# Performance work log

Hardware: AMD Instinct MI355X
Metric: run time of the kernel (lower is better)

Reference implementation:

```python
import jax, jax.numpy as jnp
import numpy as np

N_EMBD = 1024
N_HEAD = 16
B, T = 1, 4096
EPS = 1e-5


def layer_norm(x, w):
    mu = jnp.mean(x, axis=-1, keepdims=True)
    var = jnp.var(x, axis=-1, keepdims=True)
    return (x - mu) / jnp.sqrt(var + EPS) * w


def setup_inputs() -> dict:
    key = jax.random.key(0)
    ks = jax.random.split(key, 6)
    s = 0.02
    return {
        "x": jax.random.normal(ks[0], (B, T, N_EMBD), dtype=jnp.float32),
        "w_qkv": jax.random.normal(ks[1], (N_EMBD, 3 * N_EMBD), dtype=jnp.float32) * s,
        "w_attn_proj": jax.random.normal(ks[2], (N_EMBD, N_EMBD), dtype=jnp.float32) * s,
        "w_fc": jax.random.normal(ks[3], (N_EMBD, 4 * N_EMBD), dtype=jnp.float32) * s,
        "w_mlp_proj": jax.random.normal(ks[4], (4 * N_EMBD, N_EMBD), dtype=jnp.float32) * s,
        "ln1_w": jnp.ones((N_EMBD,), dtype=jnp.float32),
        "ln2_w": jnp.ones((N_EMBD,), dtype=jnp.float32),
    }


def reference(x, w_qkv, w_attn_proj, w_fc, w_mlp_proj, ln1_w, ln2_w):
    Bq, Tq, C = x.shape
    hs = C // N_HEAD

    # --- attention branch (pre-norm) ---
    h = layer_norm(x, ln1_w)
    qkv = h @ w_qkv  # [B,T,3C]
    q, k, v = jnp.split(qkv, 3, axis=-1)
    q = q.reshape(Bq, Tq, N_HEAD, hs).transpose(0, 2, 1, 3)  # [B,H,T,hs]
    k = k.reshape(Bq, Tq, N_HEAD, hs).transpose(0, 2, 1, 3)
    v = v.reshape(Bq, Tq, N_HEAD, hs).transpose(0, 2, 1, 3)

    scores = jnp.einsum("bhqd,bhkd->bhqk", q, k) * (1.0 / jnp.sqrt(jnp.float32(hs)))
    causal = jnp.tril(jnp.ones((Tq, Tq), dtype=bool))
    scores = jnp.where(causal, scores, -jnp.inf)
    weights = jax.nn.softmax(scores, axis=-1)  # dropout=0 -> identity
    out = jnp.einsum("bhqk,bhkd->bhqd", weights, v)
    out = out.transpose(0, 2, 1, 3).reshape(Bq, Tq, C)
    x = x + out @ w_attn_proj

    # --- MLP branch (pre-norm) ---
    h = layer_norm(x, ln2_w)
    h = jax.nn.gelu(h @ w_fc, approximate=False)  # nn.GELU default is exact
    x = x + h @ w_mlp_proj
    return x
```

## Files before the change

### kernel.cpp

```cpp
#include <hip/hip_runtime.h>
#include <cstdint>

typedef __attribute__((ext_vector_type(8))) short short8;
typedef __attribute__((ext_vector_type(4))) float f32x4;

__device__ __forceinline__ float b2f(unsigned short u) {
    return __uint_as_float(((unsigned int)u) << 16);
}
__device__ __forceinline__ unsigned short f2b(float f) {
    unsigned int u = __float_as_uint(f);
    u += 0x7FFFu + ((u >> 16) & 1u);
    return (unsigned short)(u >> 16);
}
__device__ __forceinline__ void gload16(const unsigned short* g, unsigned short* l) {
    __builtin_amdgcn_global_load_lds(
        (const __attribute__((address_space(1))) void*)g,
        (__attribute__((address_space(3))) void*)l, 16, 0, 0);
}

__global__ __launch_bounds__(256) void k_transpose_all(
        const float* __restrict__ w0, const float* __restrict__ w1,
        const float* __restrict__ w2, const float* __restrict__ w3,
        unsigned short* __restrict__ o0, unsigned short* __restrict__ o1,
        unsigned short* __restrict__ o2, unsigned short* __restrict__ o3) {
    __shared__ float tile[32][33];
    int b = blockIdx.x;
    const float* w; unsigned short* o; int K, N, nx, tb;
    if (b < 3072)      { w = w0; o = o0; K = 1024; N = 3072; nx = 96;  tb = b; }
    else if (b < 4096) { w = w1; o = o1; K = 1024; N = 1024; nx = 32;  tb = b - 3072; }
    else if (b < 8192) { w = w2; o = o2; K = 1024; N = 4096; nx = 128; tb = b - 4096; }
    else               { w = w3; o = o3; K = 4096; N = 1024; nx = 32;  tb = b - 8192; }
    int n0 = (tb % nx) * 32, k0 = (tb / nx) * 32;
    int tx = threadIdx.x, ty = threadIdx.y;
#pragma unroll
    for (int i = 0; i < 4; i++)
        tile[ty + 8 * i][tx] = w[(size_t)(k0 + ty + 8 * i) * N + n0 + tx];
    __syncthreads();
#pragma unroll
    for (int i = 0; i < 4; i++)
        o[(size_t)(n0 + ty + 8 * i) * K + k0 + tx] = f2b(tile[tx][ty + 8 * i]);
}

__global__ __launch_bounds__(256) void k_layernorm(
        const float* __restrict__ x, const float* __restrict__ w,
        unsigned short* __restrict__ out) {
    int row = blockIdx.x, tid = threadIdx.x;
    const float4* xr = (const float4*)(x + (size_t)row * 1024);
    float4 v = xr[tid];
    float s  = v.x + v.y + v.z + v.w;
    float ss = v.x * v.x + v.y * v.y + v.z * v.z + v.w * v.w;
#pragma unroll
    for (int off = 32; off >= 1; off >>= 1) {
        s  += __shfl_down(s, off);
        ss += __shfl_down(ss, off);
    }
    __shared__ float red[10];
    if ((tid & 63) == 0) { red[tid >> 6] = s; red[4 + (tid >> 6)] = ss; }
    __syncthreads();
    if (tid == 0) {
        float S  = red[0] + red[1] + red[2] + red[3];
        float SS = red[4] + red[5] + red[6] + red[7];
        float mu  = S * (1.0f / 1024.0f);
        float var = SS * (1.0f / 1024.0f) - mu * mu;
        red[8] = mu; red[9] = rsqrtf(var + 1e-5f);
    }
    __syncthreads();
    float mu = red[8], rs = red[9];
    float4 wv = ((const float4*)w)[tid];
    ushort4 pk;
    pk.x = f2b((v.x - mu) * rs * wv.x);
    pk.y = f2b((v.y - mu) * rs * wv.y);
    pk.z = f2b((v.z - mu) * rs * wv.z);
    pk.w = f2b((v.w - mu) * rs * wv.w);
    *(ushort4*)(out + (size_t)row * 1024 + tid * 4) = pk;
}

__global__ __launch_bounds__(256) void k_reduce_ln(
        const float* __restrict__ res, const float* __restrict__ p0,
        const float* __restrict__ p1, const float* __restrict__ w,
        float* __restrict__ xout, unsigned short* __restrict__ hout) {
    int row = blockIdx.x, tid = threadIdx.x;
    size_t i = (size_t)row * 256 + tid;
    float4 a = ((const float4*)res)[i];
    float4 b = ((const float4*)p0)[i];
    float4 c = ((const float4*)p1)[i];
    float4 v;
    v.x = a.x + b.x + c.x; v.y = a.y + b.y + c.y;
    v.z = a.z + b.z + c.z; v.w = a.w + b.w + c.w;
    ((float4*)xout)[i] = v;
    float s  = v.x + v.y + v.z + v.w;
    float ss = v.x * v.x + v.y * v.y + v.z * v.z + v.w * v.w;
#pragma unroll
    for (int off = 32; off >= 1; off >>= 1) {
        s  += __shfl_down(s, off);
        ss += __shfl_down(ss, off);
    }
    __shared__ float red[10];
    if ((tid & 63) == 0) { red[tid >> 6] = s; red[4 + (tid >> 6)] = ss; }
    __syncthreads();
    if (tid == 0) {
        float S  = red[0] + red[1] + red[2] + red[3];
        float SS = red[4] + red[5] + red[6] + red[7];
        float mu  = S * (1.0f / 1024.0f);
        float var = SS * (1.0f / 1024.0f) - mu * mu;
        red[8] = mu; red[9] = rsqrtf(var + 1e-5f);
    }
    __syncthreads();
    float mu = red[8], rs = red[9];
    float4 wv = ((const float4*)w)[tid];
    ushort4 pk;
    pk.x = f2b((v.x - mu) * rs * wv.x);
    pk.y = f2b((v.y - mu) * rs * wv.y);
    pk.z = f2b((v.z - mu) * rs * wv.z);
    pk.w = f2b((v.w - mu) * rs * wv.w);
    *(ushort4*)(hout + (size_t)row * 1024 + tid * 4) = pk;
}

__global__ __launch_bounds__(256) void k_reduce(
        const float* __restrict__ res, const float* __restrict__ p0,
        const float* __restrict__ p1, float* __restrict__ out, int n4) {
    int i = blockIdx.x * 256 + threadIdx.x;
    if (i < n4) {
        float4 a = ((const float4*)res)[i];
        float4 b = ((const float4*)p0)[i];
        float4 c = ((const float4*)p1)[i];
        a.x += b.x + c.x; a.y += b.y + c.y; a.z += b.z + c.z; a.w += b.w + c.w;
        ((float4*)out)[i] = a;
    }
}

template <int EPI, int TM, int TN, int MINW>
__global__ __launch_bounds__(256, MINW) void k_gemm_bt(
        const unsigned short* __restrict__ A, const unsigned short* __restrict__ BT,
        const float* __restrict__ RES, void* __restrict__ OUT,
        int M, int N, int K) {
    constexpr int WT = (TM == 128) ? 64 : 32;
    constexpr int MI = WT / 16;
    constexpr int NA = TM / 32, NB = TN / 32;
    __shared__ __align__(16) unsigned short As[TM * 64];
    __shared__ __align__(16) unsigned short Bs[TN * 64];
    int tid  = threadIdx.x;
    int lane = tid & 63, wave = tid >> 6;
    int quad = lane >> 4, qr = lane & 15;
    int wm_off = (wave >> 1) * WT;
    int wn_off = (wave & 1) * WT;
    int m0 = blockIdx.y * TM, n0 = blockIdx.x * TN;
    int ks = K / gridDim.z;
    int kbeg = blockIdx.z * ks;
    int r0 = tid >> 3;
    int c0 = (tid & 7) * 8;
    int cs = 8 * (((tid & 7) + (r0 & 7)) & 7);
    int cswz[2];
#pragma unroll
    for (int kk = 0; kk < 2; kk++) cswz[kk] = 8 * (((kk * 4) + quad + (qr & 7)) & 7);

    const unsigned short* Ap = A  + (size_t)(m0 + r0) * K + kbeg + c0;
    const unsigned short* Bp = BT + (size_t)(n0 + r0) * K + kbeg + c0;
    const size_t sA = (size_t)32 * K;

    uint4 pa0, pa1, pa2, pa3, pb0, pb1, pb2, pb3;
    pa0 = *(const uint4*)(Ap);
    pa1 = *(const uint4*)(Ap + sA);
    if constexpr (NA == 4) {
        pa2 = *(const uint4*)(Ap + 2 * sA);
        pa3 = *(const uint4*)(Ap + 3 * sA);
    }
    pb0 = *(const uint4*)(Bp);
    pb1 = *(const uint4*)(Bp + sA);
    if constexpr (NB == 4) {
        pb2 = *(const uint4*)(Bp + 2 * sA);
        pb3 = *(const uint4*)(Bp + 3 * sA);
    }

    f32x4 acc[MI][MI] = {};
    for (int k0 = 0; k0 < ks; k0 += 64) {
        __syncthreads();
        *(uint4*)&As[(r0)      * 64 + cs] = pa0;
        *(uint4*)&As[(32 + r0) * 64 + cs] = pa1;
        if constexpr (NA == 4) {
            *(uint4*)&As[(64 + r0) * 64 + cs] = pa2;
            *(uint4*)&As[(96 + r0) * 64 + cs] = pa3;
        }
        *(uint4*)&Bs[(r0)      * 64 + cs] = pb0;
        *(uint4*)&Bs[(32 + r0) * 64 + cs] = pb1;
        if constexpr (NB == 4) {
            *(uint4*)&Bs[(64 + r0) * 64 + cs] = pb2;
            *(uint4*)&Bs[(96 + r0) * 64 + cs] = pb3;
        }
        __syncthreads();
        if (k0 + 64 < ks) {
            int k = k0 + 64;
            pa0 = *(const uint4*)(Ap + k);
            pa1 = *(const uint4*)(Ap + sA + k);
            if constexpr (NA == 4) {
                pa2 = *(const uint4*)(Ap + 2 * sA + k);
                pa3 = *(const uint4*)(Ap + 3 * sA + k);
            }
            pb0 = *(const uint4*)(Bp + k);
            pb1 = *(const uint4*)(Bp + sA + k);
            if constexpr (NB == 4) {
                pb2 = *(const uint4*)(Bp + 2 * sA + k);
                pb3 = *(const uint4*)(Bp + 3 * sA + k);
            }
        }
#pragma unroll
        for (int kk = 0; kk < 2; kk++) {
            short8 af[MI], bfr[MI];
#pragma unroll
            for (int i = 0; i < MI; i++) af[i]  = *(const short8*)&As[(wm_off + i * 16 + qr) * 64 + cswz[kk]];
#pragma unroll
            for (int j = 0; j < MI; j++) bfr[j] = *(const short8*)&Bs[(wn_off + j * 16 + qr) * 64 + cswz[kk]];
#pragma unroll
            for (int i = 0; i < MI; i++)
#pragma unroll
                for (int j = 0; j < MI; j++)
                    acc[i][j] = __builtin_amdgcn_mfma_f32_16x16x32_bf16(af[i], bfr[j], acc[i][j], 0, 0, 0);
        }
    }
    float* outz = (EPI == 0) ? ((float*)OUT + (size_t)blockIdx.z * M * N) : (float*)OUT;
#pragma unroll
    for (int i = 0; i < MI; i++) {
#pragma unroll
        for (int j = 0; j < MI; j++) {
#pragma unroll
            for (int r = 0; r < 4; r++) {
                int row = m0 + wm_off + i * 16 + quad * 4 + r;
                int col = n0 + wn_off + j * 16 + qr;
                size_t idx = (size_t)row * N + col;
                float v = acc[i][j][r];
                if (EPI == 0)      outz[idx] = v;
                else if (EPI == 1) ((unsigned short*)OUT)[idx] = f2b(v);
                else if (EPI == 2) ((float*)OUT)[idx] = RES[idx] + v;
                else {
                    float u = v * fmaf(v * v, 0.035677408f, 0.79788456f);
                    float e = fminf(u * 2.885390082f, 80.0f);
                    float t = exp2f(e);
                    float g = v * t / (t + 1.0f);
                    ((unsigned short*)OUT)[idx] = f2b(g);
                }
            }
        }
    }
}

template <int EPI>
__global__ __launch_bounds__(512, 2) void k_gemm_8p(
        const unsigned short* __restrict__ A, const unsigned short* __restrict__ BT,
        void* __restrict__ OUT, int M, int N, int K) {
    __shared__ __align__(16) unsigned short As[2][256 * 64];
    __shared__ __align__(16) unsigned short Bs[2][256 * 64];
    int tid = threadIdx.x;
    int lane = tid & 63, wave = tid >> 6;
    int quad = lane >> 4, qr = lane & 15;
    int wr = wave >> 2, wc = wave & 3;
    int m0 = blockIdx.y * 256, n0 = blockIdx.x * 256;
    int nk = K / 64;

    int srow = tid >> 3, sblk = tid & 7;
    int scol = 8 * ((sblk - (srow & 7)) & 7);
    const unsigned short* Ag = A  + (size_t)(m0 + srow) * K + scol;
    const unsigned short* Bg = BT + (size_t)(n0 + srow) * K + scol;
    const size_t rstep = (size_t)64 * K;

    int cswz[2];
#pragma unroll
    for (int kk = 0; kk < 2; kk++) cswz[kk] = 8 * (((kk * 4) + quad + (qr & 7)) & 7);

    auto stageA = [&](int buf, int half, int kt) {
        int k = (kt < nk ? kt : 0) * 64;
#pragma unroll
        for (int rr = 0; rr < 2; rr++) {
            int r4 = half * 2 + rr;
            gload16(Ag + (size_t)r4 * rstep + k, &As[buf][r4 * 4096 + wave * 512]);
        }
    };
    auto stageB = [&](int buf, int half, int kt) {
        int k = (kt < nk ? kt : 0) * 64;
#pragma unroll
        for (int rr = 0; rr < 2; rr++) {
            int r4 = half * 2 + rr;
            gload16(Bg + (size_t)r4 * rstep + k, &Bs[buf][r4 * 4096 + wave * 512]);
        }
    };

    f32x4 acc[8][4] = {};
    stageA(0, 0, 0); stageA(0, 1, 0); stageB(0, 0, 0); stageB(0, 1, 0);
    stageA(1, 0, 1); stageA(1, 1, 1); stageB(1, 0, 1); stageB(1, 1, 1);
    asm volatile("s_waitcnt vmcnt(8)" ::: "memory");
    __builtin_amdgcn_s_barrier();

    short8 bf[4][2];
    for (int t = 0; t < nk; t += 2) {
#pragma unroll
        for (int ph = 0; ph < 8; ph++) {
            const int B = ph >> 2;
            const int p = ph & 3;
            if (p == 0) {
#pragma unroll
                for (int j = 0; j < 4; j++)
#pragma unroll
                    for (int kk = 0; kk < 2; kk++)
                        bf[j][kk] = *(const short8*)&Bs[B][(wc * 64 + j * 16 + qr) * 64 + cswz[kk]];
            }
            short8 af[2][2];
#pragma unroll
            for (int i2 = 0; i2 < 2; i2++)
#pragma unroll
                for (int kk = 0; kk < 2; kk++)
                    af[i2][kk] = *(const short8*)&As[B][(wr * 128 + (p * 2 + i2) * 16 + qr) * 64 + cswz[kk]];
            if (ph == 0)      { if (t) stageA(1, 0, t + 1); }
            else if (ph == 1) { if (t) stageA(1, 1, t + 1); stageB(0, 0, t + 2); }
            else if (ph == 2) { stageB(0, 1, t + 2); }
            else if (ph == 4) { stageA(0, 0, t + 2); }
            else if (ph == 5) { stageA(0, 1, t + 2); stageB(1, 0, t + 3); }
            else if (ph == 6) { stageB(1, 1, t + 3); }
            __builtin_amdgcn_s_barrier();
            asm volatile("s_waitcnt lgkmcnt(0)" ::: "memory");
            __builtin_amdgcn_sched_barrier(0);
            __builtin_amdgcn_s_setprio(1);
#pragma unroll
            for (int i2 = 0; i2 < 2; i2++)
#pragma unroll
                for (int kk = 0; kk < 2; kk++)
#pragma unroll
                    for (int j = 0; j < 4; j++)
                        acc[p * 2 + i2][j] = __builtin_amdgcn_mfma_f32_16x16x32_bf16(
                            af[i2][kk], bf[j][kk], acc[p * 2 + i2][j], 0, 0, 0);
            __builtin_amdgcn_s_setprio(0);
            if (p == 3) asm volatile("s_waitcnt vmcnt(4)" ::: "memory");
            __builtin_amdgcn_s_barrier();
        }
    }
    asm volatile("s_waitcnt vmcnt(0)" ::: "memory");

#pragma unroll
    for (int i = 0; i < 8; i++) {
#pragma unroll
        for (int j = 0; j < 4; j++) {
#pragma unroll
            for (int r = 0; r < 4; r++) {
                int row = m0 + wr * 128 + i * 16 + quad * 4 + r;
                int col = n0 + wc * 64 + j * 16 + qr;
                size_t idx = (size_t)row * N + col;
                float v = acc[i][j][r];
                if (EPI == 1) ((unsigned short*)OUT)[idx] = f2b(v);
                else {
                    float u = v * fmaf(v * v, 0.035677408f, 0.79788456f);
                    float e = fminf(u * 2.885390082f, 80.0f);
                    float tt = exp2f(e);
                    float g = v * tt / (tt + 1.0f);
                    ((unsigned short*)OUT)[idx] = f2b(g);
                }
            }
        }
    }
}

__global__ __launch_bounds__(256) void k_attn(
        const unsigned short* __restrict__ qkv, unsigned short* __restrict__ out) {
    __shared__ unsigned short Ks[128][72];
    __shared__ unsigned short Vt[64][136];
    __shared__ unsigned short Ps[4][16][136];

    const float C1 = 0.18033688f;
    const float C2 = 5.77078016f;

    int l = blockIdx.x;
    int h = l & 15;
    int qb = 63 - (l >> 4);
    int q0 = qb * 64;

    int tid = threadIdx.x;
    int wave = tid >> 6, lane = tid & 63;
    int lane16 = lane & 15, quad = lane >> 4;

    {
        int srow = tid >> 2, sc0 = (tid & 3) * 16;
        size_t base = (size_t)(q0 + srow) * 3072 + h * 64 + sc0;
        *(uint4*)&Ks[srow][sc0]     = *(const uint4*)&qkv[base];
        *(uint4*)&Ks[srow][sc0 + 8] = *(const uint4*)&qkv[base + 8];
    }
    __syncthreads();
    short8 aq0 = *(const short8*)&Ks[wave * 16 + lane16][quad * 8];
    short8 aq1 = *(const short8*)&Ks[wave * 16 + lane16][32 + quad * 8];

    f32x4 Oacc[4] = {};
    float l_part[4] = {0.f, 0.f, 0.f, 0.f};

    int srow = tid >> 1, sc0 = (tid & 1) * 32;
    int vk = (lane & 31) * 2;
    int d0 = wave * 16 + (lane >> 5) * 8;

    uint4 pk0, pk1, pk2, pk3, pv0, pv1, pv2, pv3;
    {
        size_t base = (size_t)srow * 3072 + 1024 + h * 64 + sc0;
        pk0 = *(const uint4*)&qkv[base];
        pk1 = *(const uint4*)&qkv[base + 8];
        pk2 = *(const uint4*)&qkv[base + 16];
        pk3 = *(const uint4*)&qkv[base + 24];
        size_t vb0 = (size_t)vk * 3072 + 2048 + h * 64 + d0;
        pv0 = *(const uint4*)&qkv[vb0];
        pv1 = *(const uint4*)&qkv[vb0 + 3072];
        size_t vb1 = (size_t)(64 + vk) * 3072 + 2048 + h * 64 + d0;
        pv2 = *(const uint4*)&qkv[vb1];
        pv3 = *(const uint4*)&qkv[vb1 + 3072];
    }

    for (int kc = 0; kc <= qb; kc += 2) {
        __syncthreads();
        {
            *(uint4*)&Ks[srow][sc0]      = pk0;
            *(uint4*)&Ks[srow][sc0 + 8]  = pk1;
            *(uint4*)&Ks[srow][sc0 + 16] = pk2;
            *(uint4*)&Ks[srow][sc0 + 24] = pk3;
        }
        {
            const unsigned short* pe0 = (const unsigned short*)&pv0;
            const unsigned short* po0 = (const unsigned short*)&pv1;
            const unsigned short* pe1 = (const unsigned short*)&pv2;
            const unsigned short* po1 = (const unsigned short*)&pv3;
#pragma unroll
            for (int j = 0; j < 8; j++) {
                *(uint32_t*)&Vt[d0 + j][vk]      = (uint32_t)pe0[j] | ((uint32_t)po0[j] << 16);
                *(uint32_t*)&Vt[d0 + j][64 + vk] = (uint32_t)pe1[j] | ((uint32_t)po1[j] << 16);
            }
        }
        __syncthreads();

        if (kc + 2 <= qb) {
            size_t base = (size_t)((kc + 2) * 64 + srow) * 3072 + 1024 + h * 64 + sc0;
            pk0 = *(const uint4*)&qkv[base];
            pk1 = *(const uint4*)&qkv[base + 8];
            pk2 = *(const uint4*)&qkv[base + 16];
            pk3 = *(const uint4*)&qkv[base + 24];
            size_t vb0 = (size_t)((kc + 2) * 64 + vk) * 3072 + 2048 + h * 64 + d0;
            pv0 = *(const uint4*)&qkv[vb0];
            pv1 = *(const uint4*)&qkv[vb0 + 3072];
            size_t vb1 = (size_t)((kc + 3) * 64 + vk) * 3072 + 2048 + h * 64 + d0;
            pv2 = *(const uint4*)&qkv[vb1];
            pv3 = *(const uint4*)&qkv[vb1 + 3072];
        }

        f32x4 sacc[8] = {};
#pragma unroll
        for (int kt = 0; kt < 8; kt++) {
            short8 bk0 = *(const short8*)&Ks[kt * 16 + lane16][quad * 8];
            short8 bk1 = *(const short8*)&Ks[kt * 16 + lane16][32 + quad * 8];
            sacc[kt] = __builtin_amdgcn_mfma_f32_16x16x32_bf16(aq0, bk0, sacc[kt], 0, 0, 0);
            sacc[kt] = __builtin_amdgcn_mfma_f32_16x16x32_bf16(aq1, bk1, sacc[kt], 0, 0, 0);
        }

        bool domask = (kc + 2 > qb);
#pragma unroll
        for (int r = 0; r < 4; r++) {
            int qrow = q0 + wave * 16 + quad * 4 + r;
#pragma unroll
            for (int kt = 0; kt < 8; kt++) {
                float s = sacc[kt][r];
                if (domask) {
                    int key = kc * 64 + kt * 16 + lane16;
                    s = (key <= qrow) ? s : -__builtin_inff();
                }
                float p = exp2f(fmaf(s, C1, -C2));
                l_part[r] += p;
                Ps[wave][quad * 4 + r][kt * 16 + lane16] =
                    (unsigned short)(__float_as_uint(p) >> 16);
            }
        }

#pragma unroll
        for (int s = 0; s < 4; s++) {
            short8 ap = *(const short8*)&Ps[wave][lane16][s * 32 + quad * 8];
#pragma unroll
            for (int dt = 0; dt < 4; dt++) {
                short8 bv = *(const short8*)&Vt[dt * 16 + lane16][s * 32 + quad * 8];
                Oacc[dt] = __builtin_amdgcn_mfma_f32_16x16x32_bf16(ap, bv, Oacc[dt], 0, 0, 0);
            }
        }
    }

    float invl[4];
#pragma unroll
    for (int r = 0; r < 4; r++) {
        float lf = l_part[r];
        lf += __shfl_xor(lf, 1);
        lf += __shfl_xor(lf, 2);
        lf += __shfl_xor(lf, 4);
        lf += __shfl_xor(lf, 8);
        invl[r] = 1.0f / lf;
    }
#pragma unroll
    for (int dt = 0; dt < 4; dt++) {
#pragma unroll
        for (int r = 0; r < 4; r++) {
            int qrow = q0 + wave * 16 + quad * 4 + r;
            out[(size_t)qrow * 1024 + h * 64 + dt * 16 + lane16] = f2b(Oacc[dt][r] * invl[r]);
        }
    }
}

extern "C" void kernel_launch(void* const* d_in, const int* in_sizes, int n_in,
                              void* d_out, int out_size, void* d_ws, size_t ws_size,
                              hipStream_t stream) {
    const float* x      = (const float*)d_in[0];
    const float* w_qkv  = (const float*)d_in[1];
    const float* w_attn = (const float*)d_in[2];
    const float* w_fc   = (const float*)d_in[3];
    const float* w_mlp  = (const float*)d_in[4];
    const float* ln1w   = (const float*)d_in[5];
    const float* ln2w   = (const float*)d_in[6];

    char* ws = (char*)d_ws;
    unsigned short* h      = (unsigned short*)(ws + 0);
    unsigned short* wqkvT  = (unsigned short*)(ws + 8388608);
    unsigned short* wattnT = (unsigned short*)(ws + 14680064);
    unsigned short* wfcT   = (unsigned short*)(ws + 16777216);
    unsigned short* wmlpT  = (unsigned short*)(ws + 25165824);
    unsigned short* qkv    = (unsigned short*)(ws + 33554432);
    unsigned short* attno  = (unsigned short*)(ws + 58720256);
    float*          x2     = (float*)(ws + 67108864);
    unsigned short* fcact  = (unsigned short*)(ws + 83886080);
    float* pA = (float*)(ws + 83886080);
    float* pM = (float*)(ws + 33554432);
    float* outF = (float*)d_out;

    k_transpose_all<<<12288, dim3(32, 8), 0, stream>>>(
        w_qkv, w_attn, w_fc, w_mlp, wqkvT, wattnT, wfcT, wmlpT);

    k_layernorm<<<4096, 256, 0, stream>>>(x, ln1w, h);
    k_gemm_8p<1><<<dim3(12, 16), 512, 0, stream>>>(h, wqkvT, qkv, 4096, 3072, 1024);
    k_attn<<<1024, 256, 0, stream>>>(qkv, attno);
    k_gemm_bt<0, 128, 128, 3><<<dim3(8, 32, 2), 256, 0, stream>>>(attno, wattnT, nullptr, pA, 4096, 1024, 1024);
    k_reduce_ln<<<4096, 256, 0, stream>>>(x, pA, pA + 4194304, ln2w, x2, h);
    k_gemm_8p<3><<<dim3(16, 16), 512, 0, stream>>>(h, wfcT, fcact, 4096, 4096, 1024);
    k_gemm_bt<0, 128, 128, 3><<<dim3(8, 32, 2), 256, 0, stream>>>(fcact, wmlpT, nullptr, pM, 4096, 1024, 4096);
    k_reduce<<<4096, 256, 0, stream>>>(x2, pM, pM + 4194304, outF, 1048576);
}
```

Baseline: 364.1 us.

## Run MLP down-projection on the 256x256 8-wave GEMM with 4-way split-K

The MLP projection GEMM (K=4096) moves from the 128x128 split-K-2 kernel to the larger 256x256 pipelined 8-wave kernel. That kernel gains a split-K mode through gridDim.z and writes fp32 partials into four buffers, which a new 4-input reduce kernel sums with the residual. The goal is better data reuse and MFMA throughput from the bigger tiles while keeping 256 blocks for occupancy. The cost is extra partial-sum traffic, since four fp32 partials are written and read instead of two. The partial buffers also reuse workspace regions and the output buffer, which relies on those regions being dead at that point in the schedule.

```diff
diff --git a/kernel.cpp b/kernel.cpp
--- a/kernel.cpp
+++ b/kernel.cpp
@@ -125,6 +125,25 @@
         float4 b = ((const float4*)p0)[i];
         float4 c = ((const float4*)p1)[i];
         a.x += b.x + c.x; a.y += b.y + c.y; a.z += b.z + c.z; a.w += b.w + c.w;
+        ((float4*)out)[i] = a;
+    }
+}
+
+__global__ __launch_bounds__(256) void k_reduce4(
+        const float* __restrict__ res, const float* __restrict__ p0,
+        const float* __restrict__ p1, const float* __restrict__ p2,
+        const float* __restrict__ p3, float* __restrict__ out, int n4) {
+    int i = blockIdx.x * 256 + threadIdx.x;
+    if (i < n4) {
+        float4 a = ((const float4*)res)[i];
+        float4 b = ((const float4*)p0)[i];
+        float4 c = ((const float4*)p1)[i];
+        float4 d = ((const float4*)p2)[i];
+        float4 e = ((const float4*)p3)[i];
+        a.x += b.x + c.x + d.x + e.x;
+        a.y += b.y + c.y + d.y + e.y;
+        a.z += b.z + c.z + d.z + e.z;
+        a.w += b.w + c.w + d.w + e.w;
         ((float4*)out)[i] = a;
     }
 }
@@ -246,7 +265,9 @@
 template <int EPI>
 __global__ __launch_bounds__(512, 2) void k_gemm_8p(
         const unsigned short* __restrict__ A, const unsigned short* __restrict__ BT,
-        void* __restrict__ OUT, int M, int N, int K) {
+        void* __restrict__ OUT, int M, int N, int K,
+        float* __restrict__ P0, float* __restrict__ P1,
+        float* __restrict__ P2, float* __restrict__ P3) {
     __shared__ __align__(16) unsigned short As[2][256 * 64];
     __shared__ __align__(16) unsigned short Bs[2][256 * 64];
     int tid = threadIdx.x;
@@ -254,12 +275,14 @@
     int quad = lane >> 4, qr = lane & 15;
     int wr = wave >> 2, wc = wave & 3;
     int m0 = blockIdx.y * 256, n0 = blockIdx.x * 256;
-    int nk = K / 64;
+    int ks = K / gridDim.z;
+    int kbeg = blockIdx.z * ks;
+    int nk = ks / 64;
 
     int srow = tid >> 3, sblk = tid & 7;
     int scol = 8 * ((sblk - (srow & 7)) & 7);
-    const unsigned short* Ag = A  + (size_t)(m0 + srow) * K + scol;
-    const unsigned short* Bg = BT + (size_t)(n0 + srow) * K + scol;
+    const unsigned short* Ag = A  + (size_t)(m0 + srow) * K + kbeg + scol;
+    const unsigned short* Bg = BT + (size_t)(n0 + srow) * K + kbeg + scol;
     const size_t rstep = (size_t)64 * K;
 
     int cswz[2];
@@ -333,6 +356,10 @@
     }
     asm volatile("s_waitcnt vmcnt(0)" ::: "memory");
 
+    float* outz = nullptr;
+    if (EPI == 0)
+        outz = (blockIdx.z == 0) ? P0 : (blockIdx.z == 1) ? P1
+             : (blockIdx.z == 2) ? P2 : P3;
 #pragma unroll
     for (int i = 0; i < 8; i++) {
 #pragma unroll
@@ -343,7 +370,8 @@
                 int col = n0 + wc * 64 + j * 16 + qr;
                 size_t idx = (size_t)row * N + col;
                 float v = acc[i][j][r];
-                if (EPI == 1) ((unsigned short*)OUT)[idx] = f2b(v);
+                if (EPI == 0)      outz[idx] = v;
+                else if (EPI == 1) ((unsigned short*)OUT)[idx] = f2b(v);
                 else {
                     float u = v * fmaf(v * v, 0.035677408f, 0.79788456f);
                     float e = fminf(u * 2.885390082f, 80.0f);
@@ -521,18 +549,24 @@
     float*          x2     = (float*)(ws + 67108864);
     unsigned short* fcact  = (unsigned short*)(ws + 83886080);
     float* pA = (float*)(ws + 83886080);
-    float* pM = (float*)(ws + 33554432);
+    float* pM0 = (float*)(ws + 33554432);
+    float* pM1 = (float*)(ws + 50331648);
+    float* pM2 = (float*)(ws + 0);
+    float* pM3 = (float*)d_out;
     float* outF = (float*)d_out;
 
     k_transpose_all<<<12288, dim3(32, 8), 0, stream>>>(
         w_qkv, w_attn, w_fc, w_mlp, wqkvT, wattnT, wfcT, wmlpT);
 
     k_layernorm<<<4096, 256, 0, stream>>>(x, ln1w, h);
-    k_gemm_8p<1><<<dim3(12, 16), 512, 0, stream>>>(h, wqkvT, qkv, 4096, 3072, 1024);
+    k_gemm_8p<1><<<dim3(12, 16), 512, 0, stream>>>(h, wqkvT, qkv, 4096, 3072, 1024,
+                                                   nullptr, nullptr, nullptr, nullptr);
     k_attn<<<1024, 256, 0, stream>>>(qkv, attno);
     k_gemm_bt<0, 128, 128, 3><<<dim3(8, 32, 2), 256, 0, stream>>>(attno, wattnT, nullptr, pA, 4096, 1024, 1024);
     k_reduce_ln<<<4096, 256, 0, stream>>>(x, pA, pA + 4194304, ln2w, x2, h);
-    k_gemm_8p<3><<<dim3(16, 16), 512, 0, stream>>>(h, wfcT, fcact, 4096, 4096, 1024);
-    k_gemm_bt<0, 128, 128, 3><<<dim3(8, 32, 2), 256, 0, stream>>>(fcact, wmlpT, nullptr, pM, 4096, 1024, 4096);
-    k_reduce<<<4096, 256, 0, stream>>>(x2, pM, pM + 4194304, outF, 1048576);
-}
+    k_gemm_8p<3><<<dim3(16, 16), 512, 0, stream>>>(h, wfcT, fcact, 4096, 4096, 1024,
+                                                   nullptr, nullptr, nullptr, nullptr);
+    k_gemm_8p<0><<<dim3(4, 16, 4), 512, 0, stream>>>(fcact, wmlpT, nullptr, 4096, 1024, 4096,
+                                                     pM0, pM1, pM2, pM3);
+    k_reduce4<<<4096, 256, 0, stream>>>(x2, pM0, pM1, pM2, pM3, outF, 1048576);
+}
```

Measured after the change: 367.7 us. About the same (+1.0%).
